# Optimization experiments

Hardware: AMD Instinct MI355X
Metric: run time of the kernel (lower is better)

Reference implementation:

```python
import jax, jax.numpy as jnp
import numpy as np

N, M = 1024, 32
FN, FE = 64, 32
AGG_N, AGG_E = 128, 64
OUT_N, OUT_E = 64, 32


def _build_indices(n, m):
    nip, eip = [], []
    k = 0
    for i in range(1, n):
        j0 = max(0, i - m)
        nip += list(range(j0, i))
        eip += list(range(k, k + i - j0))
        k += i - j0
    n1 = np.array(nip, np.int32)
    eT = np.array(eip, np.int32)
    n2 = np.concatenate([np.full(min(i, m), i, np.int32) for i in range(1, n)])
    # padded previous-node window indices (0 = zero pad slot)
    prev_nodes = np.zeros(n * m, np.int32)
    k = 0
    for i in range(n):
        t = min(i, m)
        prev_nodes[(i + 1) * m - t:(i + 1) * m] = np.arange(k, k + t) + 1
        k += t
    n_e = k
    norm_node = np.full(n, 1.0 / m, np.float32)
    for i in range(1, m):
        norm_node[i] = 1.0 / i
    prev_edges = np.zeros(n_e * m, np.int32)
    k = 0
    e = 0
    for i in range(n):
        j0 = max(0, i - m)
        for j in range(j0, i):
            if j > j0:
                prev_edges[(e + 1) * m - (j - j0):(e + 1) * m] = np.arange(k, k + j - j0) + 1
            e += 1
        k += i - j0
    norm_edge = np.ones(n_e, np.float32)
    k = 0
    for i in range(1, n):
        t = min(i, m)
        for j in range(t):
            if j > 0:
                norm_edge[k] = 1.0 / j
            k += 1
    return n1, eT, n2, prev_nodes, norm_node, prev_edges, norm_edge, n_e

N1, ET, N2, PREV_N, NORM_N, PREV_E, NORM_E, NE = _build_indices(N, M)
N1 = jnp.asarray(N1); ET = jnp.asarray(ET); N2 = jnp.asarray(N2)
PREV_N = jnp.asarray(PREV_N); PREV_E = jnp.asarray(PREV_E)
NORM_N = jnp.asarray(NORM_N); NORM_E = jnp.asarray(NORM_E)


def setup_inputs() -> dict:
    key = jax.random.key(0)
    ks = jax.random.split(key, 20)
    s = 0.02
    inp = {
        'input_nodes': jax.random.normal(ks[0], (2, N, FN), jnp.float32),
        'input_edges': jax.random.normal(ks[1], (2, NE, FE), jnp.float32),
        # node-branch MLPs (exclude_last=False)
        'Wan1': jax.random.normal(ks[2], (2 * FN + FE, 2 * AGG_N)) * s,
        'ban1': jnp.zeros((2 * AGG_N,)),
        'Wan2': jax.random.normal(ks[3], (2 * AGG_N, AGG_N)) * s,
        'ban2': jnp.zeros((AGG_N,)),
        'Wln1': jax.random.normal(ks[4], (AGG_N + FN, AGG_N + FN)) * s,
        'bln1': jnp.zeros((AGG_N + FN,)),
        'Wln2': jax.random.normal(ks[5], (AGG_N + FN, OUT_N)) * s,
        'bln2': jnp.zeros((OUT_N,)),
        # edge-branch MLPs
        'Wae1': jax.random.normal(ks[6], (FN + FE, 2 * AGG_E)) * s,
        'bae1': jnp.zeros((2 * AGG_E,)),
        'Wae2': jax.random.normal(ks[7], (2 * AGG_E, AGG_E)) * s,
        'bae2': jnp.zeros((AGG_E,)),
        'Wle1': jax.random.normal(ks[8], (AGG_E + FE, AGG_E + FE)) * s,
        'ble1': jnp.zeros((AGG_E + FE,)),
        'Wle2': jax.random.normal(ks[9], (AGG_E + FE, OUT_E)) * s,
        'ble2': jnp.zeros((OUT_E,)),
    }
    return inp


def _mlp2(x, W1, b1, W2, b2):
    return jax.nn.relu(jax.nn.relu(x @ W1 + b1) @ W2 + b2)


def reference(input_nodes, input_edges, Wan1, ban1, Wan2, ban2, Wln1, bln1, Wln2, bln2,
              Wae1, bae1, Wae2, bae2, Wle1, ble1, Wle2, ble2):
    B = input_nodes.shape[0]
    # gather node-edge pairs [B, NE, FN+FE] and node-edge-node triples [B, NE, 2FN+FE]
    pairs = jnp.concatenate([input_nodes[:, N1], input_edges[:, ET]], axis=-1)
    triples = jnp.concatenate([input_nodes[:, N1], input_edges[:, ET], input_nodes[:, N2]], axis=-1)
    # node branch (exclude_last=False -> triples)
    hn = _mlp2(triples, Wan1, ban1, Wan2, ban2)                     # [B, NE, AGG_N]
    hn = jnp.concatenate([jnp.zeros((B, 1, AGG_N), hn.dtype), hn], axis=1)
    pn = hn[:, PREV_N].reshape(B, N, M, AGG_N).sum(axis=2)          # padded window sum
    pn = pn * NORM_N[None, :, None]
    nodes_in = jnp.concatenate([pn, input_nodes], axis=-1)
    out_nodes = _mlp2(nodes_in, Wln1, bln1, Wln2, bln2)             # activation_nodes = relu
    # edge branch (pairs)
    he = _mlp2(pairs, Wae1, bae1, Wae2, bae2)                       # [B, NE, AGG_E]
    he = jnp.concatenate([jnp.zeros((B, 1, AGG_E), he.dtype), he], axis=1)
    pe = he[:, PREV_E].reshape(B, NE, M, AGG_E).sum(axis=2)
    pe = pe * NORM_E[None, :, None]
    edges_in = jnp.concatenate([pe, input_edges], axis=-1)
    out_edges = _mlp2(edges_in, Wle1, ble1, Wle2, ble2)             # activation_edges = relu
    return out_nodes, out_edges
```

## Files before the change

kernel.cpp:

```cpp
#include <hip/hip_runtime.h>
#include <cstdint>

#define NN    1024
#define MM    32
#define NEDGE 32240
#define MROWS 64480
#define PX    168
#define PST   392

typedef unsigned short ushort_t;

typedef __bf16 bf16x8 __attribute__((ext_vector_type(8)));
typedef float  floatx4 __attribute__((ext_vector_type(4)));

__device__ __forceinline__ float b2f(ushort_t u) {
    union { unsigned int i; float f; } v; v.i = ((unsigned int)u) << 16; return v.f;
}
__device__ __forceinline__ ushort_t f2b(float f) {
    unsigned int u = __builtin_bit_cast(unsigned int, f);
    u = (u + 0x7FFFu + ((u >> 16) & 1u)) >> 16;
    return (ushort_t)u;
}
__device__ __forceinline__ int edge_base(int i) {
    return (i <= MM) ? ((i * (i - 1)) >> 1) : (496 + (i - MM) * MM);
}
__device__ __forceinline__ void edge_ij(int e, int& i, int& j) {
    if (e < 496) {
        i = (int)((1.0f + sqrtf(8.0f * (float)e + 1.0f)) * 0.5f);
        while (((i * (i - 1)) >> 1) > e) --i;
        while (((i * (i + 1)) >> 1) <= e) ++i;
        j = e - ((i * (i - 1)) >> 1);
    } else {
        int q = e - 496;
        i = MM + (q >> 5);
        j = i - MM + (q & 31);
    }
}

__global__ __launch_bounds__(256) void k_pack(
        const float* an1, const float* an2, const float* ae1, const float* ae2,
        const float* le1, const float* le2, const float* ln1, const float* ln2,
        const float* nodes, const float* edges,
        ushort_t* pan1, ushort_t* pan2, ushort_t* pae1, ushort_t* pae2,
        ushort_t* ple1, ushort_t* ple2, ushort_t* pln1, ushort_t* pln2,
        ushort_t* nodesb, ushort_t* edgesb, int2* ijt) {
    __shared__ float tile[32][33];
    const int bid = blockIdx.x;
    const int tid = threadIdx.x;
    if (bid < 152) {
        const float* s; ushort_t* d; int K, N, t;
        if (bid < 40)       { s = an1; d = pan1; K = 160; N = 256; t = bid;       }
        else if (bid < 72)  { s = an2; d = pan2; K = 256; N = 128; t = bid - 40;  }
        else if (bid < 84)  { s = ae1; d = pae1; K = 96;  N = 128; t = bid - 72;  }
        else if (bid < 92)  { s = ae2; d = pae2; K = 128; N = 64;  t = bid - 84;  }
        else if (bid < 101) { s = le1; d = ple1; K = 96;  N = 96;  t = bid - 92;  }
        else if (bid < 104) { s = le2; d = ple2; K = 96;  N = 32;  t = bid - 101; }
        else if (bid < 140) { s = ln1; d = pln1; K = 192; N = 192; t = bid - 104; }
        else                { s = ln2; d = pln2; K = 192; N = 64;  t = bid - 140; }
        int ntn = N >> 5;
        int tk = t / ntn, tn = t - tk * ntn;
        int k0 = tk * 32, n0 = tn * 32;
        int tx = tid & 31, ty = tid >> 5;
#pragma unroll
        for (int m = 0; m < 4; ++m)
            tile[ty + m * 8][tx] = s[(size_t)(k0 + ty + m * 8) * N + n0 + tx];
        __syncthreads();
#pragma unroll
        for (int m = 0; m < 4; ++m)
            d[(size_t)(n0 + ty + m * 8) * K + k0 + tx] = f2b(tile[tx][ty + m * 8]);
    } else if (bid < 280) {
        int i4 = (bid - 152) * 256 + tid;
        float4 v = ((const float4*)nodes)[i4];
        uint2 o;
        o.x = (unsigned)f2b(v.x) | ((unsigned)f2b(v.y) << 16);
        o.y = (unsigned)f2b(v.z) | ((unsigned)f2b(v.w) << 16);
        ((uint2*)nodesb)[i4] = o;
    } else if (bid < 2296) {
        int i4 = (bid - 280) * 256 + tid;
        if (i4 < 515840) {
            float4 v = ((const float4*)edges)[i4];
            uint2 o;
            o.x = (unsigned)f2b(v.x) | ((unsigned)f2b(v.y) << 16);
            o.y = (unsigned)f2b(v.z) | ((unsigned)f2b(v.w) << 16);
            ((uint2*)edgesb)[i4] = o;
        }
    } else {
        int e = (bid - 2296) * 256 + tid;
        if (e < NEDGE) { int i, j; edge_ij(e, i, j); ijt[e] = make_int2(i, j); }
    }
}

__global__ __launch_bounds__(512, 2) void k_agg(
        const ushort_t* __restrict__ nodesb, const ushort_t* __restrict__ edgesb,
        const int2* __restrict__ ijt,
        const ushort_t* __restrict__ pan1, const float* __restrict__ ban1,
        const ushort_t* __restrict__ pan2, const float* __restrict__ ban2,
        const ushort_t* __restrict__ pae1, const float* __restrict__ bae1,
        const ushort_t* __restrict__ pae2, const float* __restrict__ bae2,
        ushort_t* __restrict__ hn, ushort_t* __restrict__ he) {
    __shared__ alignas(16) ushort_t X[32 * PX];
    __shared__ alignas(16) ushort_t H[32 * PST];
    const int tid = threadIdx.x;
    const int w = tid >> 6, l = tid & 63, lrow = l & 15, lq = l >> 4;
    const int mt = blockIdx.x;
    floatx4 zero = {0.f, 0.f, 0.f, 0.f};

    bf16x8 B0[5], B1[5], B2[3];
#pragma unroll
    for (int kt = 0; kt < 5; ++kt) {
        B0[kt] = *(const bf16x8*)(pan1 + (size_t)(16 * w + lrow) * 160 + kt * 32 + lq * 8);
        B1[kt] = *(const bf16x8*)(pan1 + (size_t)(16 * (w + 8) + lrow) * 160 + kt * 32 + lq * 8);
    }
#pragma unroll
    for (int kt = 0; kt < 3; ++kt)
        B2[kt] = *(const bf16x8*)(pae1 + (size_t)(16 * w + lrow) * 96 + kt * 32 + lq * 8);
    float c0 = ban1[16 * w + lrow];
    float c1 = ban1[16 * (w + 8) + lrow];
    float c2 = bae1[16 * w + lrow];

#pragma unroll
    for (int k = 0; k < 4; ++k) {
        int rr = w * 4 + k;
        int r = mt * 32 + rr;
        int off = (r >= NEDGE) ? 1 : 0;
        int2 ij = ijt[r - off * NEDGE];
        int bN = off * NN;
        unsigned* xr = (unsigned*)(X + rr * PX);
        const unsigned* nj = (const unsigned*)(nodesb + (size_t)(bN + ij.y) * 64);
        const unsigned* ni = (const unsigned*)(nodesb + (size_t)(bN + ij.x) * 64);
        const unsigned* eb = (const unsigned*)(edgesb + (size_t)r * 32);
        if (l < 32) { xr[l] = nj[l]; xr[48 + l] = ni[l]; }
        else        xr[l] = eb[l - 32];
    }
    __syncthreads();

#pragma unroll
    for (int s = 0; s < 2; ++s) {
        bf16x8 A[5];
#pragma unroll
        for (int kt = 0; kt < 5; ++kt)
            A[kt] = *(const bf16x8*)&X[(s * 16 + lrow) * PX + kt * 32 + lq * 8];
        floatx4 a0 = zero, a1 = zero, a2 = zero;
#pragma unroll
        for (int kt = 0; kt < 5; ++kt) {
            a0 = __builtin_amdgcn_mfma_f32_16x16x32_bf16(A[kt], B0[kt], a0, 0, 0, 0);
            a1 = __builtin_amdgcn_mfma_f32_16x16x32_bf16(A[kt], B1[kt], a1, 0, 0, 0);
        }
#pragma unroll
        for (int kt = 0; kt < 3; ++kt)
            a2 = __builtin_amdgcn_mfma_f32_16x16x32_bf16(A[kt], B2[kt], a2, 0, 0, 0);
#pragma unroll
        for (int r_ = 0; r_ < 4; ++r_) {
            int row = (s * 16 + lq * 4 + r_) * PST;
            H[row + 16 * w + lrow]       = f2b(fmaxf(a0[r_] + c0, 0.f));
            H[row + 128 + 16 * w + lrow] = f2b(fmaxf(a1[r_] + c1, 0.f));
            H[row + 256 + 16 * w + lrow] = f2b(fmaxf(a2[r_] + c2, 0.f));
        }
    }
    __syncthreads();

    floatx4 o0[2], o1[2];
    if (w < 4) {
        bf16x8 D0[8], D1[8];
#pragma unroll
        for (int kt = 0; kt < 8; ++kt) {
            D0[kt] = *(const bf16x8*)(pan2 + (size_t)(16 * w + lrow) * 256 + kt * 32 + lq * 8);
            D1[kt] = *(const bf16x8*)(pan2 + (size_t)(16 * (w + 4) + lrow) * 256 + kt * 32 + lq * 8);
        }
        float d0 = ban2[16 * w + lrow];
        float d1 = ban2[16 * (w + 4) + lrow];
#pragma unroll
        for (int s = 0; s < 2; ++s) {
            floatx4 a0 = zero, a1 = zero;
#pragma unroll
            for (int kt = 0; kt < 8; ++kt) {
                bf16x8 a = *(const bf16x8*)&H[(s * 16 + lrow) * PST + kt * 32 + lq * 8];
                a0 = __builtin_amdgcn_mfma_f32_16x16x32_bf16(a, D0[kt], a0, 0, 0, 0);
                a1 = __builtin_amdgcn_mfma_f32_16x16x32_bf16(a, D1[kt], a1, 0, 0, 0);
            }
#pragma unroll
            for (int r_ = 0; r_ < 4; ++r_) { o0[s][r_] = a0[r_] + d0; o1[s][r_] = a1[r_] + d1; }
        }
    } else {
        int u = w - 4;
        bf16x8 E[4];
#pragma unroll
        for (int kt = 0; kt < 4; ++kt)
            E[kt] = *(const bf16x8*)(pae2 + (size_t)(16 * u + lrow) * 128 + kt * 32 + lq * 8);
        float d2 = bae2[16 * u + lrow];
#pragma unroll
        for (int s = 0; s < 2; ++s) {
            floatx4 a2 = zero;
#pragma unroll
            for (int kt = 0; kt < 4; ++kt) {
                bf16x8 a = *(const bf16x8*)&H[(s * 16 + lrow) * PST + 256 + kt * 32 + lq * 8];
                a2 = __builtin_amdgcn_mfma_f32_16x16x32_bf16(a, E[kt], a2, 0, 0, 0);
            }
#pragma unroll
            for (int r_ = 0; r_ < 4; ++r_) o0[s][r_] = a2[r_] + d2;
        }
    }
    __syncthreads();

    ushort_t* S = X;
    ushort_t* T = H;
    if (w < 4) {
#pragma unroll
        for (int s = 0; s < 2; ++s)
#pragma unroll
            for (int r_ = 0; r_ < 4; ++r_) {
                int row = (s * 16 + lq * 4 + r_) * 136;
                S[row + 16 * w + lrow]        = f2b(fmaxf(o0[s][r_], 0.f));
                S[row + 64 + 16 * w + lrow]   = f2b(fmaxf(o1[s][r_], 0.f));
            }
    } else {
        int u = w - 4;
#pragma unroll
        for (int s = 0; s < 2; ++s)
#pragma unroll
            for (int r_ = 0; r_ < 4; ++r_)
                T[(s * 16 + lq * 4 + r_) * 72 + 16 * u + lrow] = f2b(fmaxf(o0[s][r_], 0.f));
    }
    __syncthreads();

    {
        int row = tid >> 4, c = tid & 15;
        ((uint4*)(hn + (size_t)(mt * 32 + row) * 128))[c] = *(const uint4*)&S[row * 136 + c * 8];
        if (tid < 256) {
            int row2 = tid >> 3, c2 = tid & 7;
            ((uint4*)(he + (size_t)(mt * 32 + row2) * 64))[c2] = *(const uint4*)&T[row2 * 72 + c2 * 8];
        }
    }
}

__global__ __launch_bounds__(256) void k_mid(
        const ushort_t* __restrict__ hn, const ushort_t* __restrict__ he,
        ushort_t* __restrict__ pn, ushort_t* __restrict__ pre) {
    const int tid = threadIdx.x;
    if (blockIdx.x < 2048) {
        int ri = blockIdx.x;
        int b = ri >> 10, i = ri & 1023;
        int t = min(i, MM);
        int base = b * NEDGE + edge_base(i);
        int c = tid & 63, g = tid >> 6;
        float s0 = 0.f, s1 = 0.f;
        for (int p = g; p < t; p += 4) {
            unsigned u = ((const unsigned*)(hn + (size_t)(base + p) * 128))[c];
            s0 += b2f((ushort_t)(u & 0xffff));
            s1 += b2f((ushort_t)(u >> 16));
        }
        __shared__ float red[4][128];
        red[g][c * 2] = s0; red[g][c * 2 + 1] = s1;
        __syncthreads();
        if (tid < 64) {
            float inv = 1.0f / (float)max(t, 1);
            float a0 = (red[0][tid * 2] + red[1][tid * 2] + red[2][tid * 2] + red[3][tid * 2]) * inv;
            float a1 = (red[0][tid * 2 + 1] + red[1][tid * 2 + 1] + red[2][tid * 2 + 1] + red[3][tid * 2 + 1]) * inv;
            ((unsigned*)(pn + (size_t)ri * 128))[tid] = (unsigned)f2b(a0) | ((unsigned)f2b(a1) << 16);
        }
    } else {
        int bi = blockIdx.x - 2048;
        int b = bi >> 10, i = bi & 1023;
        int t = min(i, MM);
        if (t == 0) return;
        int base = b * NEDGE + edge_base(i);
        __shared__ alignas(16) ushort_t hw[32 * 64];
        for (int u = tid; u < t * 8; u += 256)
            ((uint4*)hw)[u] = ((const uint4*)he)[(size_t)base * 8 + u];
        __syncthreads();
        if (tid < 64) {
            float run = 0.f;
            for (int p = 0; p < t; ++p) {
                float v = (p == 0) ? 0.f : run / (float)p;
                pre[(size_t)(base + p) * 64 + tid] = f2b(v);
                run += b2f(hw[p * 64 + tid]);
            }
        }
    }
}

__global__ __launch_bounds__(192) void k_final(
        const ushort_t* __restrict__ pn, const ushort_t* __restrict__ nodesb,
        const ushort_t* __restrict__ pln1, const float* __restrict__ bln1,
        const ushort_t* __restrict__ pln2, const float* __restrict__ bln2,
        float* __restrict__ out_nodes,
        const ushort_t* __restrict__ pre, const ushort_t* __restrict__ edgesb,
        const ushort_t* __restrict__ ple1, const float* __restrict__ ble1,
        const ushort_t* __restrict__ ple2, const float* __restrict__ ble2,
        float* __restrict__ out_edges) {
    __shared__ alignas(16) ushort_t LA[32 * 200];
    __shared__ alignas(16) ushort_t LB[32 * 200];
    const int tid = threadIdx.x;
    const int w = tid >> 6, l = tid & 63, lrow = l & 15, lq = l >> 4;
    floatx4 zero = {0.f, 0.f, 0.f, 0.f};

    if (blockIdx.x < 64) {
        int tile = blockIdx.x;
        for (int u = tid; u < 768; u += 192) {
            int row = u / 24, c = u - row * 24;
            int r = tile * 32 + row;
            const uint4* src = (c < 16) ? ((const uint4*)(pn + (size_t)r * 128) + c)
                                        : ((const uint4*)(nodesb + (size_t)r * 64) + (c - 16));
            *(uint4*)&LA[row * 200 + c * 8] = *src;
        }
        bf16x8 f1[6][4]; float v1[4];
#pragma unroll
        for (int kt = 0; kt < 6; ++kt)
#pragma unroll
            for (int nt = 0; nt < 4; ++nt)
                f1[kt][nt] = *(const bf16x8*)(pln1 + (size_t)(w * 64 + nt * 16 + lrow) * 192 + kt * 32 + lq * 8);
#pragma unroll
        for (int nt = 0; nt < 4; ++nt) v1[nt] = bln1[w * 64 + nt * 16 + lrow];
        __syncthreads();

        floatx4 acc[2][4];
#pragma unroll
        for (int s = 0; s < 2; ++s)
#pragma unroll
            for (int nt = 0; nt < 4; ++nt) acc[s][nt] = zero;
#pragma unroll
        for (int s = 0; s < 2; ++s)
#pragma unroll
            for (int kt = 0; kt < 6; ++kt) {
                bf16x8 a = *(const bf16x8*)&LA[(s * 16 + lrow) * 200 + kt * 32 + lq * 8];
#pragma unroll
                for (int nt = 0; nt < 4; ++nt)
                    acc[s][nt] = __builtin_amdgcn_mfma_f32_16x16x32_bf16(a, f1[kt][nt], acc[s][nt], 0, 0, 0);
            }
#pragma unroll
        for (int s = 0; s < 2; ++s)
#pragma unroll
            for (int nt = 0; nt < 4; ++nt) {
                int col = w * 64 + nt * 16 + lrow;
#pragma unroll
                for (int r_ = 0; r_ < 4; ++r_)
                    LB[(s * 16 + lq * 4 + r_) * 200 + col] = f2b(fmaxf(acc[s][nt][r_] + v1[nt], 0.f));
            }
        bf16x8 f2[6][2]; float v2[2] = {0.f, 0.f};
        if (w < 2) {
#pragma unroll
            for (int kt = 0; kt < 6; ++kt)
#pragma unroll
                for (int nt = 0; nt < 2; ++nt)
                    f2[kt][nt] = *(const bf16x8*)(pln2 + (size_t)(w * 32 + nt * 16 + lrow) * 192 + kt * 32 + lq * 8);
#pragma unroll
            for (int nt = 0; nt < 2; ++nt) v2[nt] = bln2[w * 32 + nt * 16 + lrow];
        }
        __syncthreads();
        if (w < 2) {
            floatx4 a2[2][2];
#pragma unroll
            for (int s = 0; s < 2; ++s) { a2[s][0] = zero; a2[s][1] = zero; }
#pragma unroll
            for (int s = 0; s < 2; ++s)
#pragma unroll
                for (int kt = 0; kt < 6; ++kt) {
                    bf16x8 a = *(const bf16x8*)&LB[(s * 16 + lrow) * 200 + kt * 32 + lq * 8];
#pragma unroll
                    for (int nt = 0; nt < 2; ++nt)
                        a2[s][nt] = __builtin_amdgcn_mfma_f32_16x16x32_bf16(a, f2[kt][nt], a2[s][nt], 0, 0, 0);
                }
#pragma unroll
            for (int s = 0; s < 2; ++s)
#pragma unroll
                for (int nt = 0; nt < 2; ++nt) {
                    int col = w * 32 + nt * 16 + lrow;
#pragma unroll
                    for (int r_ = 0; r_ < 4; ++r_)
                        out_nodes[(size_t)(tile * 32 + s * 16 + lq * 4 + r_) * 64 + col] =
                            fmaxf(a2[s][nt][r_] + v2[nt], 0.f);
                }
        }
    } else {
        int mt = blockIdx.x - 64;
        for (int u = tid; u < 384; u += 192) {
            int row = u / 12, c = u - row * 12;
            int r = mt * 32 + row;
            const uint4* src = (c < 8) ? ((const uint4*)(pre + (size_t)r * 64) + c)
                                       : ((const uint4*)(edgesb + (size_t)r * 32) + (c - 8));
            *(uint4*)&LA[row * 104 + c * 8] = *src;
        }
        bf16x8 fb1[3][2]; float v1[2];
#pragma unroll
        for (int kt = 0; kt < 3; ++kt)
#pragma unroll
            for (int nt = 0; nt < 2; ++nt)
                fb1[kt][nt] = *(const bf16x8*)(ple1 + (size_t)(w * 32 + nt * 16 + lrow) * 96 + kt * 32 + lq * 8);
#pragma unroll
        for (int nt = 0; nt < 2; ++nt) v1[nt] = ble1[w * 32 + nt * 16 + lrow];
        bf16x8 fb2[3]; float v2 = 0.f;
        if (w < 2) {
#pragma unroll
            for (int kt = 0; kt < 3; ++kt)
                fb2[kt] = *(const bf16x8*)(ple2 + (size_t)(w * 16 + lrow) * 96 + kt * 32 + lq * 8);
            v2 = ble2[w * 16 + lrow];
        }
        __syncthreads();

        floatx4 acc[2][2];
#pragma unroll
        for (int s = 0; s < 2; ++s) { acc[s][0] = zero; acc[s][1] = zero; }
#pragma unroll
        for (int s = 0; s < 2; ++s)
#pragma unroll
            for (int kt = 0; kt < 3; ++kt) {
                bf16x8 a = *(const bf16x8*)&LA[(s * 16 + lrow) * 104 + kt * 32 + lq * 8];
#pragma unroll
                for (int nt = 0; nt < 2; ++nt)
                    acc[s][nt] = __builtin_amdgcn_mfma_f32_16x16x32_bf16(a, fb1[kt][nt], acc[s][nt], 0, 0, 0);
            }
#pragma unroll
        for (int s = 0; s < 2; ++s)
#pragma unroll
            for (int nt = 0; nt < 2; ++nt) {
                int col = w * 32 + nt * 16 + lrow;
#pragma unroll
                for (int r_ = 0; r_ < 4; ++r_)
                    LB[(s * 16 + lq * 4 + r_) * 104 + col] = f2b(fmaxf(acc[s][nt][r_] + v1[nt], 0.f));
            }
        __syncthreads();
        if (w < 2) {
            floatx4 a2[2] = {zero, zero};
#pragma unroll
            for (int s = 0; s < 2; ++s)
#pragma unroll
                for (int kt = 0; kt < 3; ++kt) {
                    bf16x8 a = *(const bf16x8*)&LB[(s * 16 + lrow) * 104 + kt * 32 + lq * 8];
                    a2[s] = __builtin_amdgcn_mfma_f32_16x16x32_bf16(a, fb2[kt], a2[s], 0, 0, 0);
                }
#pragma unroll
            for (int s = 0; s < 2; ++s) {
                int col = w * 16 + lrow;
#pragma unroll
                for (int r_ = 0; r_ < 4; ++r_)
                    out_edges[(size_t)(mt * 32 + s * 16 + lq * 4 + r_) * 32 + col] = fmaxf(a2[s][r_] + v2, 0.f);
            }
        }
    }
}

extern "C" void kernel_launch(void* const* d_in, const int* in_sizes, int n_in,
                              void* d_out, int out_size, void* d_ws, size_t ws_size,
                              hipStream_t stream) {
    const float* nodes = (const float*)d_in[0];
    const float* edges = (const float*)d_in[1];
    const float* Wan1 = (const float*)d_in[2];  const float* ban1 = (const float*)d_in[3];
    const float* Wan2 = (const float*)d_in[4];  const float* ban2 = (const float*)d_in[5];
    const float* Wln1 = (const float*)d_in[6];  const float* bln1 = (const float*)d_in[7];
    const float* Wln2 = (const float*)d_in[8];  const float* bln2 = (const float*)d_in[9];
    const float* Wae1 = (const float*)d_in[10]; const float* bae1 = (const float*)d_in[11];
    const float* Wae2 = (const float*)d_in[12]; const float* bae2 = (const float*)d_in[13];
    const float* Wle1 = (const float*)d_in[14]; const float* ble1 = (const float*)d_in[15];
    const float* Wle2 = (const float*)d_in[16]; const float* ble2 = (const float*)d_in[17];

    char* ws = (char*)d_ws;
    size_t o = 0;
    auto alloc = [&](size_t bytes) -> void* {
        void* r = ws + o;
        o += (bytes + 255) & ~(size_t)255;
        return r;
    };
    ushort_t* hn     = (ushort_t*)alloc((size_t)MROWS * 128 * 2);
    ushort_t* he     = (ushort_t*)alloc((size_t)MROWS * 64 * 2);
    ushort_t* pre    = (ushort_t*)alloc((size_t)MROWS * 64 * 2);
    ushort_t* pn     = (ushort_t*)alloc((size_t)2048 * 128 * 2);
    ushort_t* nodesb = (ushort_t*)alloc((size_t)2 * NN * 64 * 2);
    ushort_t* edgesb = (ushort_t*)alloc((size_t)MROWS * 32 * 2);
    int2*     ijt    = (int2*)alloc((size_t)NEDGE * 8);
    ushort_t* pan1 = (ushort_t*)alloc(160 * 256 * 2);
    ushort_t* pan2 = (ushort_t*)alloc(256 * 128 * 2);
    ushort_t* pae1 = (ushort_t*)alloc(96 * 128 * 2);
    ushort_t* pae2 = (ushort_t*)alloc(128 * 64 * 2);
    ushort_t* ple1 = (ushort_t*)alloc(96 * 96 * 2);
    ushort_t* ple2 = (ushort_t*)alloc(96 * 32 * 2);
    ushort_t* pln1 = (ushort_t*)alloc(192 * 192 * 2);
    ushort_t* pln2 = (ushort_t*)alloc(192 * 64 * 2);

    float* out_nodes = (float*)d_out;
    float* out_edges = (float*)d_out + 2 * NN * 64;

    k_pack<<<2422, 256, 0, stream>>>(Wan1, Wan2, Wae1, Wae2, Wle1, Wle2, Wln1, Wln2,
                                     nodes, edges,
                                     pan1, pan2, pae1, pae2, ple1, ple2, pln1, pln2,
                                     nodesb, edgesb, ijt);
    k_agg<<<2015, 512, 0, stream>>>(nodesb, edgesb, ijt,
                                    pan1, ban1, pan2, ban2,
                                    pae1, bae1, pae2, bae2, hn, he);
    k_mid<<<4096, 256, 0, stream>>>(hn, he, pn, pre);
    k_final<<<64 + 2015, 192, 0, stream>>>(pn, nodesb, pln1, bln1, pln2, bln2, out_nodes,
                                           pre, edgesb, ple1, ble1, ple2, ble2, out_edges);

    (void)in_sizes; (void)n_in; (void)out_size; (void)ws_size;
}
```

Before: 168.1 us.

## Make k_agg persistent over four tiles with register-prefetched gathers

k_agg now processes four 32-row tiles per block instead of one. The gathered node and edge data for the next tile is prefetched into registers while the current tile computes, and X is double-buffered in shared memory. Weight fragments are reloaded per tile through an asm barrier, which trades extra L1/L2 weight reads for lower register pressure, and launch bounds are raised to allow 4 blocks per CU. The grid shrinks to about 504 blocks, which may underfill the device relative to its CU count and cut latency hiding from occupancy.

Result: slower. 178.7 us (+6.3%).

```diff
diff --git a/kernel.cpp b/kernel.cpp
--- a/kernel.cpp
+++ b/kernel.cpp
@@ -7,6 +7,8 @@
 #define MROWS 64480
 #define PX    168
 #define PST   392
+#define NTILE 2015
+#define TPB   4
 
 typedef unsigned short ushort_t;
 
@@ -90,7 +92,7 @@
     }
 }
 
-__global__ __launch_bounds__(512, 2) void k_agg(
+__global__ __launch_bounds__(512, 4) void k_agg(
         const ushort_t* __restrict__ nodesb, const ushort_t* __restrict__ edgesb,
         const int2* __restrict__ ijt,
         const ushort_t* __restrict__ pan1, const float* __restrict__ ban1,
@@ -98,137 +100,158 @@
         const ushort_t* __restrict__ pae1, const float* __restrict__ bae1,
         const ushort_t* __restrict__ pae2, const float* __restrict__ bae2,
         ushort_t* __restrict__ hn, ushort_t* __restrict__ he) {
-    __shared__ alignas(16) ushort_t X[32 * PX];
+    __shared__ alignas(16) ushort_t X[2][32 * PX];
     __shared__ alignas(16) ushort_t H[32 * PST];
+    __shared__ alignas(16) ushort_t S2[32 * 72];
     const int tid = threadIdx.x;
     const int w = tid >> 6, l = tid & 63, lrow = l & 15, lq = l >> 4;
-    const int mt = blockIdx.x;
     floatx4 zero = {0.f, 0.f, 0.f, 0.f};
 
-    bf16x8 B0[5], B1[5], B2[3];
-#pragma unroll
-    for (int kt = 0; kt < 5; ++kt) {
-        B0[kt] = *(const bf16x8*)(pan1 + (size_t)(16 * w + lrow) * 160 + kt * 32 + lq * 8);
-        B1[kt] = *(const bf16x8*)(pan1 + (size_t)(16 * (w + 8) + lrow) * 160 + kt * 32 + lq * 8);
-    }
-#pragma unroll
-    for (int kt = 0; kt < 3; ++kt)
-        B2[kt] = *(const bf16x8*)(pae1 + (size_t)(16 * w + lrow) * 96 + kt * 32 + lq * 8);
-    float c0 = ban1[16 * w + lrow];
-    float c1 = ban1[16 * (w + 8) + lrow];
-    float c2 = bae1[16 * w + lrow];
-
+    const int t0 = blockIdx.x * TPB;
+    const int t1 = min(t0 + TPB, NTILE);
+
+    const float c0 = ban1[16 * w + lrow];
+    const float c1 = ban1[16 * (w + 8) + lrow];
+    const float c2 = bae1[16 * w + lrow];
+    float d0 = 0.f, d1 = 0.f, d2 = 0.f;
+    if (w < 4) { d0 = ban2[16 * w + lrow]; d1 = ban2[16 * (w + 4) + lrow]; }
+    else       { d2 = bae2[16 * (w - 4) + lrow]; }
+
+    unsigned g0[4], g1[4];
 #pragma unroll
     for (int k = 0; k < 4; ++k) {
-        int rr = w * 4 + k;
-        int r = mt * 32 + rr;
+        int r = t0 * 32 + w * 4 + k;
         int off = (r >= NEDGE) ? 1 : 0;
         int2 ij = ijt[r - off * NEDGE];
         int bN = off * NN;
-        unsigned* xr = (unsigned*)(X + rr * PX);
         const unsigned* nj = (const unsigned*)(nodesb + (size_t)(bN + ij.y) * 64);
         const unsigned* ni = (const unsigned*)(nodesb + (size_t)(bN + ij.x) * 64);
         const unsigned* eb = (const unsigned*)(edgesb + (size_t)r * 32);
-        if (l < 32) { xr[l] = nj[l]; xr[48 + l] = ni[l]; }
-        else        xr[l] = eb[l - 32];
+        g0[k] = (l < 32) ? nj[l] : ((l < 48) ? eb[l - 32] : 0u);
+        g1[k] = (l < 32) ? ni[l] : 0u;
     }
-    __syncthreads();
-
-#pragma unroll
-    for (int s = 0; s < 2; ++s) {
-        bf16x8 A[5];
-#pragma unroll
-        for (int kt = 0; kt < 5; ++kt)
-            A[kt] = *(const bf16x8*)&X[(s * 16 + lrow) * PX + kt * 32 + lq * 8];
-        floatx4 a0 = zero, a1 = zero, a2 = zero;
+
+    int buf = 0;
+    for (int t = t0; t < t1; ++t, buf ^= 1) {
+#pragma unroll
+        for (int k = 0; k < 4; ++k) {
+            unsigned* xr = (unsigned*)(X[buf] + (w * 4 + k) * PX);
+            if (l < 48) xr[l] = g0[k];
+            if (l < 32) xr[48 + l] = g1[k];
+        }
+        __syncthreads();
+
+        unsigned n0[4], n1[4];
+        const bool more = (t + 1 < t1);
+        if (more) {
+#pragma unroll
+            for (int k = 0; k < 4; ++k) {
+                int r = (t + 1) * 32 + w * 4 + k;
+                int off = (r >= NEDGE) ? 1 : 0;
+                int2 ij = ijt[r - off * NEDGE];
+                int bN = off * NN;
+                const unsigned* nj = (const unsigned*)(nodesb + (size_t)(bN + ij.y) * 64);
+                const unsigned* ni = (const unsigned*)(nodesb + (size_t)(bN + ij.x) * 64);
+                const unsigned* eb = (const unsigned*)(edgesb + (size_t)r * 32);
+                n0[k] = (l < 32) ? nj[l] : ((l < 48) ? eb[l - 32] : 0u);
+                n1[k] = (l < 32) ? ni[l] : 0u;
+            }
+        }
+
+        const ushort_t* q_an1 = pan1; const ushort_t* q_ae1 = pae1;
+        const ushort_t* q_an2 = pan2; const ushort_t* q_ae2 = pae2;
+        asm volatile("" : "+s"(q_an1), "+s"(q_ae1), "+s"(q_an2), "+s"(q_ae2));
+
+        bf16x8 B0[5], B1[5], B2[3];
 #pragma unroll
         for (int kt = 0; kt < 5; ++kt) {
-            a0 = __builtin_amdgcn_mfma_f32_16x16x32_bf16(A[kt], B0[kt], a0, 0, 0, 0);
-            a1 = __builtin_amdgcn_mfma_f32_16x16x32_bf16(A[kt], B1[kt], a1, 0, 0, 0);
+            B0[kt] = *(const bf16x8*)(q_an1 + (size_t)(16 * w + lrow) * 160 + kt * 32 + lq * 8);
+            B1[kt] = *(const bf16x8*)(q_an1 + (size_t)(16 * (w + 8) + lrow) * 160 + kt * 32 + lq * 8);
         }
 #pragma unroll
         for (int kt = 0; kt < 3; ++kt)
-            a2 = __builtin_amdgcn_mfma_f32_16x16x32_bf16(A[kt], B2[kt], a2, 0, 0, 0);
-#pragma unroll
-        for (int r_ = 0; r_ < 4; ++r_) {
-            int row = (s * 16 + lq * 4 + r_) * PST;
-            H[row + 16 * w + lrow]       = f2b(fmaxf(a0[r_] + c0, 0.f));
-            H[row + 128 + 16 * w + lrow] = f2b(fmaxf(a1[r_] + c1, 0.f));
-            H[row + 256 + 16 * w + lrow] = f2b(fmaxf(a2[r_] + c2, 0.f));
-        }
-    }
-    __syncthreads();
-
-    floatx4 o0[2], o1[2];
-    if (w < 4) {
-        bf16x8 D0[8], D1[8];
-#pragma unroll
-        for (int kt = 0; kt < 8; ++kt) {
-            D0[kt] = *(const bf16x8*)(pan2 + (size_t)(16 * w + lrow) * 256 + kt * 32 + lq * 8);
-            D1[kt] = *(const bf16x8*)(pan2 + (size_t)(16 * (w + 4) + lrow) * 256 + kt * 32 + lq * 8);
-        }
-        float d0 = ban2[16 * w + lrow];
-        float d1 = ban2[16 * (w + 4) + lrow];
+            B2[kt] = *(const bf16x8*)(q_ae1 + (size_t)(16 * w + lrow) * 96 + kt * 32 + lq * 8);
+
 #pragma unroll
         for (int s = 0; s < 2; ++s) {
-            floatx4 a0 = zero, a1 = zero;
+            bf16x8 A[5];
+#pragma unroll
+            for (int kt = 0; kt < 5; ++kt)
+                A[kt] = *(const bf16x8*)&X[buf][(s * 16 + lrow) * PX + kt * 32 + lq * 8];
+            floatx4 a0 = zero, a1 = zero, a2 = zero;
+#pragma unroll
+            for (int kt = 0; kt < 5; ++kt) {
+                a0 = __builtin_amdgcn_mfma_f32_16x16x32_bf16(A[kt], B0[kt], a0, 0, 0, 0);
+                a1 = __builtin_amdgcn_mfma_f32_16x16x32_bf16(A[kt], B1[kt], a1, 0, 0, 0);
+            }
+#pragma unroll
+            for (int kt = 0; kt < 3; ++kt)
+                a2 = __builtin_amdgcn_mfma_f32_16x16x32_bf16(A[kt], B2[kt], a2, 0, 0, 0);
+#pragma unroll
+            for (int r_ = 0; r_ < 4; ++r_) {
+                int row = (s * 16 + lq * 4 + r_) * PST;
+                H[row + 16 * w + lrow]       = f2b(fmaxf(a0[r_] + c0, 0.f));
+                H[row + 128 + 16 * w + lrow] = f2b(fmaxf(a1[r_] + c1, 0.f));
+                H[row + 256 + 16 * w + lrow] = f2b(fmaxf(a2[r_] + c2, 0.f));
+            }
+        }
+        __syncthreads();
+
+        if (w < 4) {
+            bf16x8 D0[8], D1[8];
 #pragma unroll
             for (int kt = 0; kt < 8; ++kt) {
-                bf16x8 a = *(const bf16x8*)&H[(s * 16 + lrow) * PST + kt * 32 + lq * 8];
-                a0 = __builtin_amdgcn_mfma_f32_16x16x32_bf16(a, D0[kt], a0, 0, 0, 0);
-                a1 = __builtin_amdgcn_mfma_f32_16x16x32_bf16(a, D1[kt], a1, 0, 0, 0);
-            }
-#pragma unroll
-            for (int r_ = 0; r_ < 4; ++r_) { o0[s][r_] = a0[r_] + d0; o1[s][r_] = a1[r_] + d1; }
-        }
-    } else {
-        int u = w - 4;
-        bf16x8 E[4];
-#pragma unroll
-        for (int kt = 0; kt < 4; ++kt)
-            E[kt] = *(const bf16x8*)(pae2 + (size_t)(16 * u + lrow) * 128 + kt * 32 + lq * 8);
-        float d2 = bae2[16 * u + lrow];
-#pragma unroll
-        for (int s = 0; s < 2; ++s) {
-            floatx4 a2 = zero;
-#pragma unroll
-            for (int kt = 0; kt < 4; ++kt) {
-                bf16x8 a = *(const bf16x8*)&H[(s * 16 + lrow) * PST + 256 + kt * 32 + lq * 8];
-                a2 = __builtin_amdgcn_mfma_f32_16x16x32_bf16(a, E[kt], a2, 0, 0, 0);
-            }
-#pragma unroll
-            for (int r_ = 0; r_ < 4; ++r_) o0[s][r_] = a2[r_] + d2;
-        }
-    }
-    __syncthreads();
-
-    ushort_t* S = X;
-    ushort_t* T = H;
-    if (w < 4) {
-#pragma unroll
-        for (int s = 0; s < 2; ++s)
-#pragma unroll
-            for (int r_ = 0; r_ < 4; ++r_) {
-                int row = (s * 16 + lq * 4 + r_) * 136;
-                S[row + 16 * w + lrow]        = f2b(fmaxf(o0[s][r_], 0.f));
-                S[row + 64 + 16 * w + lrow]   = f2b(fmaxf(o1[s][r_], 0.f));
-            }
-    } else {
-        int u = w - 4;
-#pragma unroll
-        for (int s = 0; s < 2; ++s)
-#pragma unroll
-            for (int r_ = 0; r_ < 4; ++r_)
-                T[(s * 16 + lq * 4 + r_) * 72 + 16 * u + lrow] = f2b(fmaxf(o0[s][r_], 0.f));
-    }
-    __syncthreads();
-
-    {
-        int row = tid >> 4, c = tid & 15;
-        ((uint4*)(hn + (size_t)(mt * 32 + row) * 128))[c] = *(const uint4*)&S[row * 136 + c * 8];
-        if (tid < 256) {
-            int row2 = tid >> 3, c2 = tid & 7;
-            ((uint4*)(he + (size_t)(mt * 32 + row2) * 64))[c2] = *(const uint4*)&T[row2 * 72 + c2 * 8];
+                D0[kt] = *(const bf16x8*)(q_an2 + (size_t)(16 * w + lrow) * 256 + kt * 32 + lq * 8);
+                D1[kt] = *(const bf16x8*)(q_an2 + (size_t)(16 * (w + 4) + lrow) * 256 + kt * 32 + lq * 8);
+            }
+#pragma unroll
+            for (int s = 0; s < 2; ++s) {
+                floatx4 a0 = zero, a1 = zero;
+#pragma unroll
+                for (int kt = 0; kt < 8; ++kt) {
+                    bf16x8 a = *(const bf16x8*)&H[(s * 16 + lrow) * PST + kt * 32 + lq * 8];
+                    a0 = __builtin_amdgcn_mfma_f32_16x16x32_bf16(a, D0[kt], a0, 0, 0, 0);
+                    a1 = __builtin_amdgcn_mfma_f32_16x16x32_bf16(a, D1[kt], a1, 0, 0, 0);
+                }
+#pragma unroll
+                for (int r_ = 0; r_ < 4; ++r_) {
+                    int row = (s * 16 + lq * 4 + r_) * 136;
+                    X[buf][row + 16 * w + lrow]      = f2b(fmaxf(a0[r_] + d0, 0.f));
+                    X[buf][row + 64 + 16 * w + lrow] = f2b(fmaxf(a1[r_] + d1, 0.f));
+                }
+            }
+        } else {
+            int u = w - 4;
+            bf16x8 E[4];
+#pragma unroll
+            for (int kt = 0; kt < 4; ++kt)
+                E[kt] = *(const bf16x8*)(q_ae2 + (size_t)(16 * u + lrow) * 128 + kt * 32 + lq * 8);
+#pragma unroll
+            for (int s = 0; s < 2; ++s) {
+                floatx4 a2 = zero;
+#pragma unroll
+                for (int kt = 0; kt < 4; ++kt) {
+                    bf16x8 a = *(const bf16x8*)&H[(s * 16 + lrow) * PST + 256 + kt * 32 + lq * 8];
+                    a2 = __builtin_amdgcn_mfma_f32_16x16x32_bf16(a, E[kt], a2, 0, 0, 0);
+                }
+#pragma unroll
+                for (int r_ = 0; r_ < 4; ++r_)
+                    S2[(s * 16 + lq * 4 + r_) * 72 + 16 * u + lrow] = f2b(fmaxf(a2[r_] + d2, 0.f));
+            }
+        }
+        __syncthreads();
+
+        {
+            int row = tid >> 4, c = tid & 15;
+            ((uint4*)(hn + (size_t)(t * 32 + row) * 128))[c] = *(const uint4*)&X[buf][row * 136 + c * 8];
+            if (tid < 256) {
+                int row2 = tid >> 3, c2 = tid & 7;
+                ((uint4*)(he + (size_t)(t * 32 + row2) * 64))[c2] = *(const uint4*)&S2[row2 * 72 + c2 * 8];
+            }
+        }
+        if (more) {
+#pragma unroll
+            for (int k = 0; k < 4; ++k) { g0[k] = n0[k]; g1[k] = n1[k]; }
         }
     }
 }
@@ -483,7 +506,7 @@
                                      nodes, edges,
                                      pan1, pan2, pae1, pae2, ple1, ple2, pln1, pln2,
                                      nodesb, edgesb, ijt);
-    k_agg<<<2015, 512, 0, stream>>>(nodesb, edgesb, ijt,
+    k_agg<<<(NTILE + TPB - 1) / TPB, 512, 0, stream>>>(nodesb, edgesb, ijt,
                                     pan1, ban1, pan2, ban2,
                                     pae1, bae1, pae2, bae2, hn, he);
     k_mid<<<4096, 256, 0, stream>>>(hn, he, pn, pre);
```
